# Optimization experiments

Measured on AMD Instinct MI355X. Metric: run time of the kernel, lower is better.

The kernel has to match this reference:

```python
import jax, jax.numpy as jnp
import numpy as np

B, NV, NP, D, K = 8, 2048, 4096, 64, 8  # shapes per batch, vtx/pts counts, feat dim, num_interp
NEG = -1e9


def _unit(x):
    return x / jnp.clip(jnp.linalg.norm(x, axis=-1, keepdims=True), 1e-12)


def _gather(v, idx):
    # v: [B, N, C], idx: [B, Q, K] -> [B, Q, K, C]
    return jax.vmap(lambda a, i: a[i])(v, idx)


def setup_inputs() -> dict:
    key = jax.random.key(0)
    k1, k2, k3, k4, k5 = jax.random.split(key, 5)
    return {
        "vtx": jax.random.normal(k1, (B * NV, 3), jnp.float32),
        "pts": jax.random.normal(k2, (B * NP, 3), jnp.float32),
        "vtx_feature": jax.random.normal(k3, (B * NV, D), jnp.float32),
        "pts_feature": jax.random.normal(k4, (B * NP, D), jnp.float32),
        "vismask_logits": jax.random.normal(k5, (B * NV, 1), jnp.float32),
    }


def reference(vtx, pts, vtx_feature, pts_feature, vismask_logits):
    # --- per-batch min-max normalization of sigmoid(vismask) (serial loop in torch) ---
    vm = jax.nn.sigmoid(vismask_logits).reshape(B, NV, 1)
    vmin = vm.min(axis=1, keepdims=True)
    vmax = vm.max(axis=1, keepdims=True)
    vm = (vm - vmin) / (vmax - vmin)

    vtxb = vtx.reshape(B, NV, 3)
    ptsb = pts.reshape(B, NP, 3)
    vf = vtx_feature.reshape(B, NV, D)
    pf = pts_feature.reshape(B, NP, D)

    # --- cosine KNN: for each vtx, k nearest pts by cosine similarity ---
    sim = jnp.einsum('bnd,bmd->bnm', _unit(vf), _unit(pf))  # [B,NV,NP]
    _, idx = jax.lax.top_k(sim, K)                           # [B,NV,K]

    nbr_pts = _gather(ptsb, idx)                             # [B,NV,K,3]
    nbr_pf = _gather(pf, idx)                                # [B,NV,K,D]
    euclid = nbr_pts - vtxb[:, :, None, :]
    # raw (unnormalized) dot product, weighted by vismask of the query vertex
    fsim = jnp.sum(nbr_pf * vf[:, :, None, :], axis=-1, keepdims=True) * vm[:, :, None, :]
    # scatter_add over assign_index[0] == sum over the K grouped neighbors
    flow_init = jnp.sum(euclid * fsim, axis=2) / jnp.sum(fsim, axis=2)  # [B,NV,3]

    # --- interpolate flow at invisible vertices from visible ones (2nd cosine KNN) ---
    vis = vm >= 0.5                                          # [B,NV,1]
    vfn = _unit(vf)
    sim2 = jnp.einsum('bnd,bmd->bnm', vfn, vfn)              # [B,NV,NV]
    sim2 = jnp.where(vis[:, :, 0][:, None, :], sim2, NEG)    # keys restricted to visible vtx
    _, idx2 = jax.lax.top_k(sim2, K)                         # [B,NV,K]

    nbr_vf = _gather(vf, idx2)                               # [B,NV,K,D]
    nbr_flow = _gather(flow_init, idx2)                      # [B,NV,K,3]
    fsim2 = jnp.sum(nbr_vf * vf[:, :, None, :], axis=-1, keepdims=True)
    invis_flow = jnp.sum(nbr_flow * fsim2, axis=2) / jnp.sum(fsim2, axis=2)

    flow = jnp.where(vis, flow_init, invis_flow)             # flow_init[invis] = invis_flow
    l1_points = jnp.concatenate([flow, vm], axis=-1)         # [B,NV,4]
    return l1_points.reshape(B * NV, 4)
```

## Files before the change

kernel.cpp:

```cpp
#include <hip/hip_runtime.h>
#include <math.h>

#define BB 8
#define NVV 2048
#define NPP 4096
#define DD 64
#define NQ (BB * NVV)
#define QT (NQ / 16)

typedef __attribute__((ext_vector_type(8))) short short8;
typedef __attribute__((ext_vector_type(8))) unsigned short ushort8;
typedef __attribute__((ext_vector_type(4))) float f32x4;


__device__ __forceinline__ unsigned short bf16rn(float x) {
  unsigned u = __float_as_uint(x);
  return (unsigned short)((u + 0x7FFFu + ((u >> 16) & 1u)) >> 16);
}
__device__ __forceinline__ float bf2f(unsigned short h) {
  return __uint_as_float(((unsigned)h) << 16);
}

__device__ __forceinline__ void net8(unsigned* a, unsigned v) {
#pragma unroll
  for (int k = 0; k < 7; k++) {
    unsigned r;
    asm("v_med3_u32 %0, %1, %2, %3" : "=v"(r) : "v"(v), "v"(a[k]), "v"(a[k + 1]));
    a[k] = r;
  }
  a[7] = a[7] > v ? a[7] : v;
}

__device__ __forceinline__ float dot64(const float4* __restrict__ a,
                                       const float4* __restrict__ b) {
  float a0 = 0.f, a1 = 0.f, a2 = 0.f, a3 = 0.f;
#pragma unroll
  for (int c = 0; c < 16; c++) {
    float4 x = a[c], y = b[c];
    a0 = fmaf(x.x, y.x, a0);
    a1 = fmaf(x.y, y.y, a1);
    a2 = fmaf(x.z, y.z, a2);
    a3 = fmaf(x.w, y.w, a3);
  }
  return (a0 + a1) + (a2 + a3);
}

__device__ __forceinline__ unsigned fkey(float s) {
  unsigned u = __float_as_uint(s);
  return ((int)u < 0) ? ~u : (u | 0x80000000u);
}

__global__ __launch_bounds__(256) void k_prep(const float* __restrict__ logits,
                                              const float* __restrict__ vf,
                                              const float* __restrict__ pf,
                                              float* __restrict__ vm,
                                              float* __restrict__ inv_vf_s,
                                              float* __restrict__ inv_pf_s,
                                              unsigned short* __restrict__ vfh,
                                              unsigned short* __restrict__ vfl,
                                              unsigned short* __restrict__ pfh,
                                              unsigned short* __restrict__ pfl,
                                              float* __restrict__ out) {
  int bid = blockIdx.x, t = threadIdx.x;
  if (bid < BB) {
    int b = bid;
    __shared__ float smn[4], smx[4];
    float vals[8];
    float mn = 1e30f, mx = -1e30f;
#pragma unroll
    for (int i = 0; i < 8; i++) {
      float x = logits[b * NVV + t + i * 256];
      float s = 1.0f / (1.0f + expf(-x));
      vals[i] = s;
      mn = fminf(mn, s);
      mx = fmaxf(mx, s);
    }
    for (int o = 32; o; o >>= 1) {
      mn = fminf(mn, __shfl_xor(mn, o, 64));
      mx = fmaxf(mx, __shfl_xor(mx, o, 64));
    }
    int w = t >> 6;
    if ((t & 63) == 0) { smn[w] = mn; smx[w] = mx; }
    __syncthreads();
    mn = fminf(fminf(smn[0], smn[1]), fminf(smn[2], smn[3]));
    mx = fmaxf(fmaxf(smx[0], smx[1]), fmaxf(smx[2], smx[3]));
    float range = mx - mn;
#pragma unroll
    for (int i = 0; i < 8; i++) {
      float v = (vals[i] - mn) / range;
      int g = b * NVV + t + i * 256;
      vm[g] = v;
      out[g * 4 + 3] = v;
    }
  } else {
    int tile_g = (bid - BB) * 4 + (t >> 6);
    int lane = t & 63, c = lane & 15, quad = (lane >> 4) & 3;
    const float* src;
    unsigned short *dh, *dl;
    float* ginv;
    int tile;
    if (tile_g < QT) { tile = tile_g; src = vf; dh = vfh; dl = vfl; ginv = inv_vf_s; }
    else { tile = tile_g - QT; src = pf; dh = pfh; dl = pfl; ginv = inv_pf_s; }
    int row = tile * 16 + c;
    const float* rp = src + (size_t)row * DD + quad * 8;
    float4 a0 = *(const float4*)(rp);
    float4 b0 = *(const float4*)(rp + 4);
    float4 a1 = *(const float4*)(rp + 32);
    float4 b1 = *(const float4*)(rp + 36);
    float xs[16] = {a0.x, a0.y, a0.z, a0.w, b0.x, b0.y, b0.z, b0.w,
                    a1.x, a1.y, a1.z, a1.w, b1.x, b1.y, b1.z, b1.w};
    float ss = 0.f;
#pragma unroll
    for (int j = 0; j < 16; j++) ss = fmaf(xs[j], xs[j], ss);
    ss += __shfl_xor(ss, 16, 64);
    ss += __shfl_xor(ss, 32, 64);
    float inv = 1.0f / fmaxf(sqrtf(ss), 1e-12f);
    if (quad == 0) ginv[row] = 16384.0f * inv;
    ushort8 h, l;
    size_t s0 = (size_t)tile * 128 + lane;
#pragma unroll
    for (int j = 0; j < 8; j++) {
      float xn = xs[j] * inv;
      unsigned short hj = bf16rn(xn);
      h[j] = hj;
      l[j] = bf16rn(xn - bf2f(hj));
    }
    *(ushort8*)(dh + s0 * 8) = h;
    *(ushort8*)(dl + s0 * 8) = l;
#pragma unroll
    for (int j = 0; j < 8; j++) {
      float xn = xs[8 + j] * inv;
      unsigned short hj = bf16rn(xn);
      h[j] = hj;
      l[j] = bf16rn(xn - bf2f(hj));
    }
    *(ushort8*)(dh + (s0 + 64) * 8) = h;
    *(ushort8*)(dl + (s0 + 64) * 8) = l;
  }
}

#define LOADK(d0, d1, d2, d3, KH, KL, tile) do {            \
    size_t bo_ = (size_t)(tile) * 1024 + lane * 8;          \
    d0 = *(const short8*)((KH) + bo_);                      \
    d1 = *(const short8*)((KH) + bo_ + 512);                \
    d2 = *(const short8*)((KL) + bo_);                      \
    d3 = *(const short8*)((KL) + bo_ + 512);                \
  } while (0)

#define MFMA6(c_, h0_, h1_, l0_, l1_) do {                                  \
    c_ = __builtin_amdgcn_mfma_f32_16x16x32_bf16(h0_, qh0, c_, 0, 0, 0);    \
    c_ = __builtin_amdgcn_mfma_f32_16x16x32_bf16(h1_, qh1, c_, 0, 0, 0);    \
    c_ = __builtin_amdgcn_mfma_f32_16x16x32_bf16(h0_, ql0, c_, 0, 0, 0);    \
    c_ = __builtin_amdgcn_mfma_f32_16x16x32_bf16(h1_, ql1, c_, 0, 0, 0);    \
    c_ = __builtin_amdgcn_mfma_f32_16x16x32_bf16(l0_, qh0, c_, 0, 0, 0);    \
    c_ = __builtin_amdgcn_mfma_f32_16x16x32_bf16(l1_, qh1, c_, 0, 0, 0);    \
  } while (0)

#define COMP1(h0_, h1_, l0_, l1_, b16_) do {                                \
    f32x4 c_ = {0.f, 0.f, 0.f, 0.f};                                        \
    MFMA6(c_, h0_, h1_, l0_, l1_);                                          \
    unsigned u0_ = (unsigned)fmaxf(fmaf(c_[0], 520000.0f, 520000.0f), 0.0f);\
    net8(tvA, (u0_ << 12) | (unsigned)((b16_) + 0));                        \
    unsigned u1_ = (unsigned)fmaxf(fmaf(c_[1], 520000.0f, 520000.0f), 0.0f);\
    net8(tvA, (u1_ << 12) | (unsigned)((b16_) + 1));                        \
    unsigned u2_ = (unsigned)fmaxf(fmaf(c_[2], 520000.0f, 520000.0f), 0.0f);\
    net8(tvB, (u2_ << 12) | (unsigned)((b16_) + 2));                        \
    unsigned u3_ = (unsigned)fmaxf(fmaf(c_[3], 520000.0f, 520000.0f), 0.0f);\
    net8(tvB, (u3_ << 12) | (unsigned)((b16_) + 3));                        \
  } while (0)

#define COMP2(h0_, h1_, l0_, l1_, b16_, mp_) do {                           \
    float4 mv_ = *(const float4*)(mp_);                                     \
    f32x4 c_ = {0.f, 0.f, 0.f, 0.f};                                        \
    MFMA6(c_, h0_, h1_, l0_, l1_);                                          \
    unsigned u0_ = (unsigned)fmaxf(fmaf(c_[0], 520000.0f, 520000.0f), 0.0f);\
    unsigned p0_ = (u0_ << 12) | (unsigned)((b16_) + 0);                    \
    net8(tvA, (mv_.x >= 0.5f) ? p0_ : 0u);                                  \
    unsigned u1_ = (unsigned)fmaxf(fmaf(c_[1], 520000.0f, 520000.0f), 0.0f);\
    unsigned p1_ = (u1_ << 12) | (unsigned)((b16_) + 1);                    \
    net8(tvA, (mv_.y >= 0.5f) ? p1_ : 0u);                                  \
    unsigned u2_ = (unsigned)fmaxf(fmaf(c_[2], 520000.0f, 520000.0f), 0.0f);\
    unsigned p2_ = (u2_ << 12) | (unsigned)((b16_) + 2);                    \
    net8(tvB, (mv_.z >= 0.5f) ? p2_ : 0u);                                  \
    unsigned u3_ = (unsigned)fmaxf(fmaf(c_[3], 520000.0f, 520000.0f), 0.0f);\
    unsigned p3_ = (u3_ << 12) | (unsigned)((b16_) + 3);                    \
    net8(tvB, (mv_.w >= 0.5f) ? p3_ : 0u);                                  \
  } while (0)

__global__ __launch_bounds__(256)
void k_knn(const unsigned short* __restrict__ vfh, const unsigned short* __restrict__ vfl,
           const unsigned short* __restrict__ pfh, const unsigned short* __restrict__ pfl,
           const float* __restrict__ vm, unsigned* __restrict__ pc2,
           const float* __restrict__ vf, const float* __restrict__ pf,
           const float* __restrict__ pts, const float* __restrict__ vtx,
           const float* __restrict__ inv_pf_s,
           float* __restrict__ flow_ws, float* __restrict__ out) {
  __shared__ unsigned mg[2][2][16][8];
  __shared__ unsigned cand[16][16];

  int p = blockIdx.x;
  int xcd = p & 7, j = p >> 3;
  int qt_g = xcd * 128 + j;
  int batch = xcd;
  int w = (int)threadIdx.x >> 6;
  int ck = w >> 1, hf = w & 1;
  int lane = threadIdx.x & 63, col = lane & 15, quad = lane >> 4;

  size_t ab = (size_t)qt_g * 1024 + lane * 8;
  short8 qh0 = *(const short8*)(vfh + ab);
  short8 qh1 = *(const short8*)(vfh + ab + 512);
  short8 ql0 = *(const short8*)(vfl + ab);
  short8 ql1 = *(const short8*)(vfl + ab + 512);
  asm volatile("" : "+a"(qh0), "+a"(qh1), "+a"(ql0), "+a"(ql1));

  unsigned tvA[8], tvB[8];

#pragma unroll
  for (int k = 0; k < 8; k++) { tvA[k] = 0u; tvB[k] = 0u; }
  {
    int bt0 = batch * 256 + ck * 128 + hf * 64;
    int tb16 = (ck * 128 + hf * 64) * 16 + quad * 4;
    short8 ah0, ah1, al0, al1, bh0, bh1, bl0, bl1;
    LOADK(ah0, ah1, al0, al1, pfh, pfl, bt0);
#pragma unroll 1
    for (int kt = 0; kt < 62; kt += 2) {
      LOADK(bh0, bh1, bl0, bl1, pfh, pfl, bt0 + kt + 1);
      COMP1(ah0, ah1, al0, al1, tb16 + kt * 16);
      LOADK(ah0, ah1, al0, al1, pfh, pfl, bt0 + kt + 2);
      COMP1(bh0, bh1, bl0, bl1, tb16 + (kt + 1) * 16);
    }
    LOADK(bh0, bh1, bl0, bl1, pfh, pfl, bt0 + 63);
    COMP1(ah0, ah1, al0, al1, tb16 + 62 * 16);
    COMP1(bh0, bh1, bl0, bl1, tb16 + 63 * 16);
  }
#pragma unroll
  for (int k = 0; k < 8; k++) net8(tvA, tvB[k]);
#pragma unroll
  for (int m = 16; m <= 32; m <<= 1) {
    unsigned ov[8];
#pragma unroll
    for (int k = 0; k < 8; k++) ov[k] = (unsigned)__shfl_xor((int)tvA[k], m, 64);
#pragma unroll
    for (int k = 7; k >= 0; k--) net8(tvA, ov[k]);
  }
  if (hf == 1 && quad == 0) {
#pragma unroll
    for (int k = 0; k < 8; k++) mg[0][ck][col][k] = tvA[k];
  }
  __syncthreads();
  if (hf == 0 && quad == 0) {
#pragma unroll
    for (int k = 0; k < 8; k++) net8(tvA, mg[0][ck][col][k]);
#pragma unroll
    for (int k = 0; k < 8; k++)
      cand[col][ck * 8 + k] = tvA[k];
  }
  __syncthreads();

  {
    int t = (int)threadIdx.x;
    int qloc = t >> 4, c = t & 15;
    int q = qt_g * 16 + qloc;
    int base = lane & 48;

    unsigned pk = cand[qloc][c];
    int id = (int)(pk & 0xFFFu);
    int prow = batch * NPP + id;
    const float4* qp = (const float4*)(vf + (size_t)q * DD);
    float dotv = dot64(qp, (const float4*)(pf + (size_t)prow * DD));
    float s = dotv * inv_pf_s[prow];
    unsigned kb = fkey(s);

    int rank = 0;
#pragma unroll
    for (int i = 0; i < 16; i++) {
      unsigned ok = (unsigned)__shfl((int)kb, base + i, 64);
      int oid = __shfl(id, base + i, 64);
      rank += (ok > kb || (ok == kb && oid > id)) ? 1 : 0;
    }
    float wgt = (rank < 8) ? dotv : 0.0f;

    float ax = (pts[prow * 3 + 0] - vtx[q * 3 + 0]) * wgt;
    float ay = (pts[prow * 3 + 1] - vtx[q * 3 + 1]) * wgt;
    float az = (pts[prow * 3 + 2] - vtx[q * 3 + 2]) * wgt;
    float den = wgt;
#pragma unroll
    for (int m = 1; m <= 8; m <<= 1) {
      ax += __shfl_xor(ax, m, 64);
      ay += __shfl_xor(ay, m, 64);
      az += __shfl_xor(az, m, 64);
      den += __shfl_xor(den, m, 64);
    }
    if (c == 0) {
      float fx = ax / den, fy = ay / den, fz = az / den;
      flow_ws[q * 4 + 0] = fx;
      flow_ws[q * 4 + 1] = fy;
      flow_ws[q * 4 + 2] = fz;
      out[q * 4 + 0] = fx;
      out[q * 4 + 1] = fy;
      out[q * 4 + 2] = fz;
    }
  }

#pragma unroll
  for (int k = 0; k < 8; k++) { tvA[k] = 0u; tvB[k] = 0u; }
  {
    const float* mask = vm + batch * NVV;
    int bt0 = batch * 128 + ck * 64 + hf * 32;
    int tbase = ck * 64 + hf * 32;
    int tb16 = tbase * 16 + quad * 4;
    const float* mp0 = mask + tbase * 16 + quad * 4;
    short8 ah0, ah1, al0, al1, bh0, bh1, bl0, bl1;
    LOADK(ah0, ah1, al0, al1, vfh, vfl, bt0);
#pragma unroll 1
    for (int kt = 0; kt < 30; kt += 2) {
      LOADK(bh0, bh1, bl0, bl1, vfh, vfl, bt0 + kt + 1);
      COMP2(ah0, ah1, al0, al1, tb16 + kt * 16, mp0 + kt * 16);
      LOADK(ah0, ah1, al0, al1, vfh, vfl, bt0 + kt + 2);
      COMP2(bh0, bh1, bl0, bl1, tb16 + (kt + 1) * 16, mp0 + (kt + 1) * 16);
    }
    LOADK(bh0, bh1, bl0, bl1, vfh, vfl, bt0 + 31);
    COMP2(ah0, ah1, al0, al1, tb16 + 30 * 16, mp0 + 30 * 16);
    COMP2(bh0, bh1, bl0, bl1, tb16 + 31 * 16, mp0 + 31 * 16);
  }
#pragma unroll
  for (int k = 0; k < 8; k++) net8(tvA, tvB[k]);
#pragma unroll
  for (int m = 16; m <= 32; m <<= 1) {
    unsigned ov[8];
#pragma unroll
    for (int k = 0; k < 8; k++) ov[k] = (unsigned)__shfl_xor((int)tvA[k], m, 64);
#pragma unroll
    for (int k = 7; k >= 0; k--) net8(tvA, ov[k]);
  }
  if (hf == 1 && quad == 0) {
#pragma unroll
    for (int k = 0; k < 8; k++) mg[1][ck][col][k] = tvA[k];
  }
  __syncthreads();
  if (hf == 0 && quad == 0) {
#pragma unroll
    for (int k = 0; k < 8; k++) net8(tvA, mg[1][ck][col][k]);
    int q = qt_g * 16 + col;
#pragma unroll
    for (int k = 0; k < 8; k++)
      pc2[(size_t)(ck * 8 + k) * NQ + q] = tvA[k];
  }
}

__global__ __launch_bounds__(256) void k_merge_final(const unsigned* __restrict__ pc,
                                                     const float* __restrict__ vf,
                                                     const float* __restrict__ vm,
                                                     const float* __restrict__ inv_vf_s,
                                                     const float* __restrict__ flow_ws,
                                                     float* __restrict__ out) {
  int p = blockIdx.x;
  int xcd = p & 7, jj = p >> 3;
  int lb = xcd * 128 + jj;
  int T = lb * 256 + (int)threadIdx.x;
  int q = T >> 4, c = T & 15, batch = q >> 11;
  if (vm[q] >= 0.5f) return;
  int lane = (int)threadIdx.x & 63;
  int base = lane & 48;

  unsigned pk = pc[(size_t)c * NQ + q];
  bool valid = pk > 0xFFFu;
  int id = (int)(pk & 0xFFFu);
  int krow = batch * NVV + id;
  const float4* qp = (const float4*)(vf + (size_t)q * DD);
  float dotv = dot64(qp, (const float4*)(vf + (size_t)krow * DD));
  float s = dotv * inv_vf_s[krow];
  unsigned kb = valid ? fkey(s) : 0u;

  int rank = 0;
#pragma unroll
  for (int i = 0; i < 16; i++) {
    unsigned ok = (unsigned)__shfl((int)kb, base + i, 64);
    int oid = __shfl(id, base + i, 64);
    rank += (ok > kb || (ok == kb && oid > id)) ? 1 : 0;
  }
  float wgt = (valid && rank < 8) ? dotv : 0.0f;

  float ax = flow_ws[krow * 4 + 0] * wgt;
  float ay = flow_ws[krow * 4 + 1] * wgt;
  float az = flow_ws[krow * 4 + 2] * wgt;
  float den = wgt;
#pragma unroll
  for (int m = 1; m <= 8; m <<= 1) {
    ax += __shfl_xor(ax, m, 64);
    ay += __shfl_xor(ay, m, 64);
    az += __shfl_xor(az, m, 64);
    den += __shfl_xor(den, m, 64);
  }
  if (c == 0) {
    out[q * 4 + 0] = ax / den;
    out[q * 4 + 1] = ay / den;
    out[q * 4 + 2] = az / den;
  }
}

extern "C" void kernel_launch(void* const* d_in, const int* in_sizes, int n_in,
                              void* d_out, int out_size, void* d_ws, size_t ws_size,
                              hipStream_t stream) {
  const float* vtx = (const float*)d_in[0];
  const float* pts = (const float*)d_in[1];
  const float* vf = (const float*)d_in[2];
  const float* pf = (const float*)d_in[3];
  const float* lg = (const float*)d_in[4];
  float* out = (float*)d_out;
  float* ws = (float*)d_ws;

  float* vm = ws;
  float* inv_vf_s = ws + 16384;
  float* inv_pf_s = ws + 32768;
  float* flow = ws + 65536;
  unsigned* pc2 = (unsigned*)(ws + 393216);
  unsigned short* vfh = (unsigned short*)(ws + 655360);
  unsigned short* vfl = (unsigned short*)(ws + 1179648);
  unsigned short* pfh = (unsigned short*)(ws + 1703936);
  unsigned short* pfl = (unsigned short*)(ws + 2752512);

  k_prep<<<BB + 768, 256, 0, stream>>>(lg, vf, pf, vm, inv_vf_s, inv_pf_s,
                                       vfh, vfl, pfh, pfl, out);
  k_knn<<<1024, 256, 0, stream>>>(vfh, vfl, pfh, pfl, vm, pc2,
                                  vf, pf, pts, vtx, inv_pf_s, flow, out);
  k_merge_final<<<NQ * 16 / 256, 256, 0, stream>>>(pc2, vf, vm, inv_vf_s,
                                                   flow, out);
}
```

Measured before the change: 163.9 us.

## Fuse prep, KNN and merge kernels into one persistent kernel with grid barriers

Replaces the three kernel launches with a single 512-block persistent kernel. Global atomic-counter barriers separate the normalization/bf16 staging phase, the KNN phase and the invisible-vertex interpolation phase. Each block now handles two query tiles, and the second-KNN candidates stay in shared memory instead of round-tripping through a global buffer. This removes launch gaps and the pc2 traffic, but it adds spin-barrier cost and relies on all 512 blocks being co-resident. It also halves the grid, which may lower parallelism in the KNN phase.

```diff
diff --git a/kernel.cpp b/kernel.cpp
--- a/kernel.cpp
+++ b/kernel.cpp
@@ -50,93 +50,57 @@
   return ((int)u < 0) ? ~u : (u | 0x80000000u);
 }
 
-__global__ __launch_bounds__(256) void k_prep(const float* __restrict__ logits,
-                                              const float* __restrict__ vf,
-                                              const float* __restrict__ pf,
-                                              float* __restrict__ vm,
-                                              float* __restrict__ inv_vf_s,
-                                              float* __restrict__ inv_pf_s,
-                                              unsigned short* __restrict__ vfh,
-                                              unsigned short* __restrict__ vfl,
-                                              unsigned short* __restrict__ pfh,
-                                              unsigned short* __restrict__ pfl,
-                                              float* __restrict__ out) {
-  int bid = blockIdx.x, t = threadIdx.x;
-  if (bid < BB) {
-    int b = bid;
-    __shared__ float smn[4], smx[4];
-    float vals[8];
-    float mn = 1e30f, mx = -1e30f;
-#pragma unroll
-    for (int i = 0; i < 8; i++) {
-      float x = logits[b * NVV + t + i * 256];
-      float s = 1.0f / (1.0f + expf(-x));
-      vals[i] = s;
-      mn = fminf(mn, s);
-      mx = fmaxf(mx, s);
-    }
-    for (int o = 32; o; o >>= 1) {
-      mn = fminf(mn, __shfl_xor(mn, o, 64));
-      mx = fmaxf(mx, __shfl_xor(mx, o, 64));
-    }
-    int w = t >> 6;
-    if ((t & 63) == 0) { smn[w] = mn; smx[w] = mx; }
-    __syncthreads();
-    mn = fminf(fminf(smn[0], smn[1]), fminf(smn[2], smn[3]));
-    mx = fmaxf(fmaxf(smx[0], smx[1]), fmaxf(smx[2], smx[3]));
-    float range = mx - mn;
-#pragma unroll
-    for (int i = 0; i < 8; i++) {
-      float v = (vals[i] - mn) / range;
-      int g = b * NVV + t + i * 256;
-      vm[g] = v;
-      out[g * 4 + 3] = v;
-    }
-  } else {
-    int tile_g = (bid - BB) * 4 + (t >> 6);
-    int lane = t & 63, c = lane & 15, quad = (lane >> 4) & 3;
-    const float* src;
-    unsigned short *dh, *dl;
-    float* ginv;
-    int tile;
-    if (tile_g < QT) { tile = tile_g; src = vf; dh = vfh; dl = vfl; ginv = inv_vf_s; }
-    else { tile = tile_g - QT; src = pf; dh = pfh; dl = pfl; ginv = inv_pf_s; }
-    int row = tile * 16 + c;
-    const float* rp = src + (size_t)row * DD + quad * 8;
-    float4 a0 = *(const float4*)(rp);
-    float4 b0 = *(const float4*)(rp + 4);
-    float4 a1 = *(const float4*)(rp + 32);
-    float4 b1 = *(const float4*)(rp + 36);
-    float xs[16] = {a0.x, a0.y, a0.z, a0.w, b0.x, b0.y, b0.z, b0.w,
-                    a1.x, a1.y, a1.z, a1.w, b1.x, b1.y, b1.z, b1.w};
-    float ss = 0.f;
-#pragma unroll
-    for (int j = 0; j < 16; j++) ss = fmaf(xs[j], xs[j], ss);
-    ss += __shfl_xor(ss, 16, 64);
-    ss += __shfl_xor(ss, 32, 64);
-    float inv = 1.0f / fmaxf(sqrtf(ss), 1e-12f);
-    if (quad == 0) ginv[row] = 16384.0f * inv;
-    ushort8 h, l;
-    size_t s0 = (size_t)tile * 128 + lane;
-#pragma unroll
-    for (int j = 0; j < 8; j++) {
-      float xn = xs[j] * inv;
-      unsigned short hj = bf16rn(xn);
-      h[j] = hj;
-      l[j] = bf16rn(xn - bf2f(hj));
-    }
-    *(ushort8*)(dh + s0 * 8) = h;
-    *(ushort8*)(dl + s0 * 8) = l;
-#pragma unroll
-    for (int j = 0; j < 8; j++) {
-      float xn = xs[8 + j] * inv;
-      unsigned short hj = bf16rn(xn);
-      h[j] = hj;
-      l[j] = bf16rn(xn - bf2f(hj));
-    }
-    *(ushort8*)(dh + (s0 + 64) * 8) = h;
-    *(ushort8*)(dl + (s0 + 64) * 8) = l;
-  }
+__device__ __forceinline__ void gridbar(unsigned* sem, unsigned target) {
+  __syncthreads();
+  __threadfence();
+  if (threadIdx.x == 0) {
+    atomicAdd(sem, 1u);
+    while (atomicAdd(sem, 0u) < target) __builtin_amdgcn_s_sleep(8);
+  }
+  __syncthreads();
+  __threadfence();
+}
+
+__device__ __forceinline__ void stage_tile(const float* __restrict__ src, int tile,
+                                           unsigned short* __restrict__ dh,
+                                           unsigned short* __restrict__ dl,
+                                           float* __restrict__ ginv, int lane) {
+  int c = lane & 15, quad = (lane >> 4) & 3;
+  int row = tile * 16 + c;
+  const float* rp = src + (size_t)row * DD + quad * 8;
+  float4 a0 = *(const float4*)(rp);
+  float4 b0 = *(const float4*)(rp + 4);
+  float4 a1 = *(const float4*)(rp + 32);
+  float4 b1 = *(const float4*)(rp + 36);
+  float xs[16] = {a0.x, a0.y, a0.z, a0.w, b0.x, b0.y, b0.z, b0.w,
+                  a1.x, a1.y, a1.z, a1.w, b1.x, b1.y, b1.z, b1.w};
+  float ss = 0.f;
+#pragma unroll
+  for (int j = 0; j < 16; j++) ss = fmaf(xs[j], xs[j], ss);
+  ss += __shfl_xor(ss, 16, 64);
+  ss += __shfl_xor(ss, 32, 64);
+  float inv = 1.0f / fmaxf(sqrtf(ss), 1e-12f);
+  if (quad == 0) ginv[row] = 16384.0f * inv;
+  ushort8 h, l;
+  size_t s0 = (size_t)tile * 128 + lane;
+#pragma unroll
+  for (int j = 0; j < 8; j++) {
+    float xn = xs[j] * inv;
+    unsigned short hj = bf16rn(xn);
+    h[j] = hj;
+    l[j] = bf16rn(xn - bf2f(hj));
+  }
+  *(ushort8*)(dh + s0 * 8) = h;
+  *(ushort8*)(dl + s0 * 8) = l;
+#pragma unroll
+  for (int j = 0; j < 8; j++) {
+    float xn = xs[8 + j] * inv;
+    unsigned short hj = bf16rn(xn);
+    h[j] = hj;
+    l[j] = bf16rn(xn - bf2f(hj));
+  }
+  *(ushort8*)(dh + (s0 + 64) * 8) = h;
+  *(ushort8*)(dl + (s0 + 64) * 8) = l;
 }
 
 #define LOADK(d0, d1, d2, d3, KH, KL, tile) do {            \
@@ -187,89 +151,234 @@
     net8(tvB, (mv_.w >= 0.5f) ? p3_ : 0u);                                  \
   } while (0)
 
-__global__ __launch_bounds__(256)
-void k_knn(const unsigned short* __restrict__ vfh, const unsigned short* __restrict__ vfl,
-           const unsigned short* __restrict__ pfh, const unsigned short* __restrict__ pfl,
-           const float* __restrict__ vm, unsigned* __restrict__ pc2,
+__global__ __launch_bounds__(256, 4)
+void k_all(const float* __restrict__ vtx, const float* __restrict__ pts,
            const float* __restrict__ vf, const float* __restrict__ pf,
-           const float* __restrict__ pts, const float* __restrict__ vtx,
-           const float* __restrict__ inv_pf_s,
-           float* __restrict__ flow_ws, float* __restrict__ out) {
+           const float* __restrict__ lg, float* __restrict__ out,
+           float* __restrict__ vm, float* __restrict__ inv_vf_s,
+           float* __restrict__ inv_pf_s, float* __restrict__ flow_ws,
+           unsigned short* __restrict__ vfh, unsigned short* __restrict__ vfl,
+           unsigned short* __restrict__ pfh, unsigned short* __restrict__ pfl,
+           unsigned* __restrict__ sem) {
+  __shared__ float smn[2], smx[2];
   __shared__ unsigned mg[2][2][16][8];
   __shared__ unsigned cand[16][16];
+  __shared__ unsigned cand2[2][16][16];
 
   int p = blockIdx.x;
-  int xcd = p & 7, j = p >> 3;
-  int qt_g = xcd * 128 + j;
+  int xcd = p & 7, idx = p >> 3;
   int batch = xcd;
-  int w = (int)threadIdx.x >> 6;
+  int t = (int)threadIdx.x;
+  int w = t >> 6;
   int ck = w >> 1, hf = w & 1;
-  int lane = threadIdx.x & 63, col = lane & 15, quad = lane >> 4;
-
-  size_t ab = (size_t)qt_g * 1024 + lane * 8;
-  short8 qh0 = *(const short8*)(vfh + ab);
-  short8 qh1 = *(const short8*)(vfh + ab + 512);
-  short8 ql0 = *(const short8*)(vfl + ab);
-  short8 ql1 = *(const short8*)(vfl + ab + 512);
-  asm volatile("" : "+a"(qh0), "+a"(qh1), "+a"(ql0), "+a"(ql1));
-
-  unsigned tvA[8], tvB[8];
-
-#pragma unroll
-  for (int k = 0; k < 8; k++) { tvA[k] = 0u; tvB[k] = 0u; }
-  {
-    int bt0 = batch * 256 + ck * 128 + hf * 64;
-    int tb16 = (ck * 128 + hf * 64) * 16 + quad * 4;
-    short8 ah0, ah1, al0, al1, bh0, bh1, bl0, bl1;
-    LOADK(ah0, ah1, al0, al1, pfh, pfl, bt0);
+  int lane = t & 63, col = lane & 15, quad = lane >> 4;
+
+  stage_tile(pf, xcd * 256 + idx * 4 + w, pfh, pfl, inv_pf_s, lane);
+  bool dovm = (idx == 0 && w >= 2);
+  float vals[16];
+  if (w < 2) stage_tile(vf, xcd * 128 + idx * 2 + w, vfh, vfl, inv_vf_s, lane);
+  float mn = 1e30f, mx = -1e30f;
+  if (dovm) {
+    int t2 = t - 128;
+#pragma unroll
+    for (int i = 0; i < 16; i++) {
+      float x = lg[batch * NVV + t2 + i * 128];
+      float s = 1.0f / (1.0f + expf(-x));
+      vals[i] = s;
+      mn = fminf(mn, s);
+      mx = fmaxf(mx, s);
+    }
+    for (int o = 32; o; o >>= 1) {
+      mn = fminf(mn, __shfl_xor(mn, o, 64));
+      mx = fmaxf(mx, __shfl_xor(mx, o, 64));
+    }
+    if (lane == 0) { smn[w - 2] = mn; smx[w - 2] = mx; }
+  }
+  __syncthreads();
+  if (dovm) {
+    int t2 = t - 128;
+    float mnn = fminf(smn[0], smn[1]), mxx = fmaxf(smx[0], smx[1]);
+    float range = mxx - mnn;
+#pragma unroll
+    for (int i = 0; i < 16; i++) {
+      float v = (vals[i] - mnn) / range;
+      int g = batch * NVV + t2 + i * 128;
+      vm[g] = v;
+      out[g * 4 + 3] = v;
+    }
+  }
+
+  gridbar(sem, 512);
+
 #pragma unroll 1
-    for (int kt = 0; kt < 62; kt += 2) {
-      LOADK(bh0, bh1, bl0, bl1, pfh, pfl, bt0 + kt + 1);
-      COMP1(ah0, ah1, al0, al1, tb16 + kt * 16);
-      LOADK(ah0, ah1, al0, al1, pfh, pfl, bt0 + kt + 2);
-      COMP1(bh0, bh1, bl0, bl1, tb16 + (kt + 1) * 16);
-    }
-    LOADK(bh0, bh1, bl0, bl1, pfh, pfl, bt0 + 63);
-    COMP1(ah0, ah1, al0, al1, tb16 + 62 * 16);
-    COMP1(bh0, bh1, bl0, bl1, tb16 + 63 * 16);
-  }
-#pragma unroll
-  for (int k = 0; k < 8; k++) net8(tvA, tvB[k]);
-#pragma unroll
-  for (int m = 16; m <= 32; m <<= 1) {
-    unsigned ov[8];
-#pragma unroll
-    for (int k = 0; k < 8; k++) ov[k] = (unsigned)__shfl_xor((int)tvA[k], m, 64);
-#pragma unroll
-    for (int k = 7; k >= 0; k--) net8(tvA, ov[k]);
-  }
-  if (hf == 1 && quad == 0) {
-#pragma unroll
-    for (int k = 0; k < 8; k++) mg[0][ck][col][k] = tvA[k];
-  }
-  __syncthreads();
-  if (hf == 0 && quad == 0) {
-#pragma unroll
-    for (int k = 0; k < 8; k++) net8(tvA, mg[0][ck][col][k]);
-#pragma unroll
-    for (int k = 0; k < 8; k++)
-      cand[col][ck * 8 + k] = tvA[k];
-  }
-  __syncthreads();
-
-  {
-    int t = (int)threadIdx.x;
+  for (int qi = 0; qi < 2; qi++) {
+    int qt_g = xcd * 128 + idx * 2 + qi;
+
+    size_t ab = (size_t)qt_g * 1024 + lane * 8;
+    short8 qh0 = *(const short8*)(vfh + ab);
+    short8 qh1 = *(const short8*)(vfh + ab + 512);
+    short8 ql0 = *(const short8*)(vfl + ab);
+    short8 ql1 = *(const short8*)(vfl + ab + 512);
+    asm volatile("" : "+a"(qh0), "+a"(qh1), "+a"(ql0), "+a"(ql1));
+
+    unsigned tvA[8], tvB[8];
+
+#pragma unroll
+    for (int k = 0; k < 8; k++) { tvA[k] = 0u; tvB[k] = 0u; }
+    {
+      int bt0 = batch * 256 + ck * 128 + hf * 64;
+      int tb16 = (ck * 128 + hf * 64) * 16 + quad * 4;
+      short8 ah0, ah1, al0, al1, bh0, bh1, bl0, bl1;
+      LOADK(ah0, ah1, al0, al1, pfh, pfl, bt0);
+#pragma unroll 1
+      for (int kt = 0; kt < 62; kt += 2) {
+        LOADK(bh0, bh1, bl0, bl1, pfh, pfl, bt0 + kt + 1);
+        COMP1(ah0, ah1, al0, al1, tb16 + kt * 16);
+        LOADK(ah0, ah1, al0, al1, pfh, pfl, bt0 + kt + 2);
+        COMP1(bh0, bh1, bl0, bl1, tb16 + (kt + 1) * 16);
+      }
+      LOADK(bh0, bh1, bl0, bl1, pfh, pfl, bt0 + 63);
+      COMP1(ah0, ah1, al0, al1, tb16 + 62 * 16);
+      COMP1(bh0, bh1, bl0, bl1, tb16 + 63 * 16);
+    }
+#pragma unroll
+    for (int k = 0; k < 8; k++) net8(tvA, tvB[k]);
+#pragma unroll
+    for (int m = 16; m <= 32; m <<= 1) {
+      unsigned ov[8];
+#pragma unroll
+      for (int k = 0; k < 8; k++) ov[k] = (unsigned)__shfl_xor((int)tvA[k], m, 64);
+#pragma unroll
+      for (int k = 7; k >= 0; k--) net8(tvA, ov[k]);
+    }
+    if (hf == 1 && quad == 0) {
+#pragma unroll
+      for (int k = 0; k < 8; k++) mg[0][ck][col][k] = tvA[k];
+    }
+    __syncthreads();
+    if (hf == 0 && quad == 0) {
+#pragma unroll
+      for (int k = 0; k < 8; k++) net8(tvA, mg[0][ck][col][k]);
+#pragma unroll
+      for (int k = 0; k < 8; k++)
+        cand[col][ck * 8 + k] = tvA[k];
+    }
+
+#pragma unroll
+    for (int k = 0; k < 8; k++) { tvA[k] = 0u; tvB[k] = 0u; }
+    {
+      const float* mask = vm + batch * NVV;
+      int bt0 = batch * 128 + ck * 64 + hf * 32;
+      int tbase = ck * 64 + hf * 32;
+      int tb16 = tbase * 16 + quad * 4;
+      const float* mp0 = mask + tbase * 16 + quad * 4;
+      short8 ah0, ah1, al0, al1, bh0, bh1, bl0, bl1;
+      LOADK(ah0, ah1, al0, al1, vfh, vfl, bt0);
+#pragma unroll 1
+      for (int kt = 0; kt < 30; kt += 2) {
+        LOADK(bh0, bh1, bl0, bl1, vfh, vfl, bt0 + kt + 1);
+        COMP2(ah0, ah1, al0, al1, tb16 + kt * 16, mp0 + kt * 16);
+        LOADK(ah0, ah1, al0, al1, vfh, vfl, bt0 + kt + 2);
+        COMP2(bh0, bh1, bl0, bl1, tb16 + (kt + 1) * 16, mp0 + (kt + 1) * 16);
+      }
+      LOADK(bh0, bh1, bl0, bl1, vfh, vfl, bt0 + 31);
+      COMP2(ah0, ah1, al0, al1, tb16 + 30 * 16, mp0 + 30 * 16);
+      COMP2(bh0, bh1, bl0, bl1, tb16 + 31 * 16, mp0 + 31 * 16);
+    }
+#pragma unroll
+    for (int k = 0; k < 8; k++) net8(tvA, tvB[k]);
+#pragma unroll
+    for (int m = 16; m <= 32; m <<= 1) {
+      unsigned ov[8];
+#pragma unroll
+      for (int k = 0; k < 8; k++) ov[k] = (unsigned)__shfl_xor((int)tvA[k], m, 64);
+#pragma unroll
+      for (int k = 7; k >= 0; k--) net8(tvA, ov[k]);
+    }
+    if (hf == 1 && quad == 0) {
+#pragma unroll
+      for (int k = 0; k < 8; k++) mg[1][ck][col][k] = tvA[k];
+    }
+    __syncthreads();
+    if (hf == 0 && quad == 0) {
+#pragma unroll
+      for (int k = 0; k < 8; k++) net8(tvA, mg[1][ck][col][k]);
+#pragma unroll
+      for (int k = 0; k < 8; k++)
+        cand2[qi][col][ck * 8 + k] = tvA[k];
+    }
+    __syncthreads();
+
+    {
+      int qloc = t >> 4, c = t & 15;
+      int q = qt_g * 16 + qloc;
+      int base = lane & 48;
+
+      unsigned pk = cand[qloc][c];
+      int id = (int)(pk & 0xFFFu);
+      int prow = batch * NPP + id;
+      const float4* qp = (const float4*)(vf + (size_t)q * DD);
+      float dotv = dot64(qp, (const float4*)(pf + (size_t)prow * DD));
+      float s = dotv * inv_pf_s[prow];
+      unsigned kb = fkey(s);
+
+      int rank = 0;
+#pragma unroll
+      for (int i = 0; i < 16; i++) {
+        unsigned ok = (unsigned)__shfl((int)kb, base + i, 64);
+        int oid = __shfl(id, base + i, 64);
+        rank += (ok > kb || (ok == kb && oid > id)) ? 1 : 0;
+      }
+      float wgt = (rank < 8) ? dotv : 0.0f;
+
+      float ax = 0.f, ay = 0.f, az = 0.f, den = 0.f;
+      if (wgt != 0.0f) {
+        ax = (pts[prow * 3 + 0] - vtx[q * 3 + 0]) * wgt;
+        ay = (pts[prow * 3 + 1] - vtx[q * 3 + 1]) * wgt;
+        az = (pts[prow * 3 + 2] - vtx[q * 3 + 2]) * wgt;
+        den = wgt;
+      }
+#pragma unroll
+      for (int m = 1; m <= 8; m <<= 1) {
+        ax += __shfl_xor(ax, m, 64);
+        ay += __shfl_xor(ay, m, 64);
+        az += __shfl_xor(az, m, 64);
+        den += __shfl_xor(den, m, 64);
+      }
+      if (c == 0) {
+        float fx = ax / den, fy = ay / den, fz = az / den;
+        flow_ws[q * 4 + 0] = fx;
+        flow_ws[q * 4 + 1] = fy;
+        flow_ws[q * 4 + 2] = fz;
+        out[q * 4 + 0] = fx;
+        out[q * 4 + 1] = fy;
+        out[q * 4 + 2] = fz;
+      }
+    }
+    __syncthreads();
+  }
+
+  gridbar(sem, 1024);
+
+#pragma unroll 1
+  for (int qi = 0; qi < 2; qi++) {
+    int lb = xcd * 128 + idx * 2 + qi;
     int qloc = t >> 4, c = t & 15;
-    int q = qt_g * 16 + qloc;
+    int q = lb * 16 + qloc;
     int base = lane & 48;
-
-    unsigned pk = cand[qloc][c];
+    bool act = vm[q] < 0.5f;
+
+    unsigned pk = cand2[qi][qloc][c];
+    bool valid = act && (pk > 0xFFFu);
     int id = (int)(pk & 0xFFFu);
-    int prow = batch * NPP + id;
-    const float4* qp = (const float4*)(vf + (size_t)q * DD);
-    float dotv = dot64(qp, (const float4*)(pf + (size_t)prow * DD));
-    float s = dotv * inv_pf_s[prow];
-    unsigned kb = fkey(s);
+    int krow = batch * NVV + id;
+    float dotv = 0.f;
+    unsigned kb = 0u;
+    if (valid) {
+      dotv = dot64((const float4*)(vf + (size_t)q * DD),
+                   (const float4*)(vf + (size_t)krow * DD));
+      kb = fkey(dotv * inv_vf_s[krow]);
+    }
 
     int rank = 0;
 #pragma unroll
@@ -278,12 +387,15 @@
       int oid = __shfl(id, base + i, 64);
       rank += (ok > kb || (ok == kb && oid > id)) ? 1 : 0;
     }
-    float wgt = (rank < 8) ? dotv : 0.0f;
-
-    float ax = (pts[prow * 3 + 0] - vtx[q * 3 + 0]) * wgt;
-    float ay = (pts[prow * 3 + 1] - vtx[q * 3 + 1]) * wgt;
-    float az = (pts[prow * 3 + 2] - vtx[q * 3 + 2]) * wgt;
-    float den = wgt;
+    float wgt = (valid && rank < 8) ? dotv : 0.0f;
+
+    float ax = 0.f, ay = 0.f, az = 0.f, den = 0.f;
+    if (wgt != 0.0f) {
+      ax = flow_ws[krow * 4 + 0] * wgt;
+      ay = flow_ws[krow * 4 + 1] * wgt;
+      az = flow_ws[krow * 4 + 2] * wgt;
+      den = wgt;
+    }
 #pragma unroll
     for (int m = 1; m <= 8; m <<= 1) {
       ax += __shfl_xor(ax, m, 64);
@@ -291,111 +403,11 @@
       az += __shfl_xor(az, m, 64);
       den += __shfl_xor(den, m, 64);
     }
-    if (c == 0) {
-      float fx = ax / den, fy = ay / den, fz = az / den;
-      flow_ws[q * 4 + 0] = fx;
-      flow_ws[q * 4 + 1] = fy;
-      flow_ws[q * 4 + 2] = fz;
-      out[q * 4 + 0] = fx;
-      out[q * 4 + 1] = fy;
-      out[q * 4 + 2] = fz;
-    }
-  }
-
-#pragma unroll
-  for (int k = 0; k < 8; k++) { tvA[k] = 0u; tvB[k] = 0u; }
-  {
-    const float* mask = vm + batch * NVV;
-    int bt0 = batch * 128 + ck * 64 + hf * 32;
-    int tbase = ck * 64 + hf * 32;
-    int tb16 = tbase * 16 + quad * 4;
-    const float* mp0 = mask + tbase * 16 + quad * 4;
-    short8 ah0, ah1, al0, al1, bh0, bh1, bl0, bl1;
-    LOADK(ah0, ah1, al0, al1, vfh, vfl, bt0);
-#pragma unroll 1
-    for (int kt = 0; kt < 30; kt += 2) {
-      LOADK(bh0, bh1, bl0, bl1, vfh, vfl, bt0 + kt + 1);
-      COMP2(ah0, ah1, al0, al1, tb16 + kt * 16, mp0 + kt * 16);
-      LOADK(ah0, ah1, al0, al1, vfh, vfl, bt0 + kt + 2);
-      COMP2(bh0, bh1, bl0, bl1, tb16 + (kt + 1) * 16, mp0 + (kt + 1) * 16);
-    }
-    LOADK(bh0, bh1, bl0, bl1, vfh, vfl, bt0 + 31);
-    COMP2(ah0, ah1, al0, al1, tb16 + 30 * 16, mp0 + 30 * 16);
-    COMP2(bh0, bh1, bl0, bl1, tb16 + 31 * 16, mp0 + 31 * 16);
-  }
-#pragma unroll
-  for (int k = 0; k < 8; k++) net8(tvA, tvB[k]);
-#pragma unroll
-  for (int m = 16; m <= 32; m <<= 1) {
-    unsigned ov[8];
-#pragma unroll
-    for (int k = 0; k < 8; k++) ov[k] = (unsigned)__shfl_xor((int)tvA[k], m, 64);
-#pragma unroll
-    for (int k = 7; k >= 0; k--) net8(tvA, ov[k]);
-  }
-  if (hf == 1 && quad == 0) {
-#pragma unroll
-    for (int k = 0; k < 8; k++) mg[1][ck][col][k] = tvA[k];
-  }
-  __syncthreads();
-  if (hf == 0 && quad == 0) {
-#pragma unroll
-    for (int k = 0; k < 8; k++) net8(tvA, mg[1][ck][col][k]);
-    int q = qt_g * 16 + col;
-#pragma unroll
-    for (int k = 0; k < 8; k++)
-      pc2[(size_t)(ck * 8 + k) * NQ + q] = tvA[k];
-  }
-}
-
-__global__ __launch_bounds__(256) void k_merge_final(const unsigned* __restrict__ pc,
-                                                     const float* __restrict__ vf,
-                                                     const float* __restrict__ vm,
-                                                     const float* __restrict__ inv_vf_s,
-                                                     const float* __restrict__ flow_ws,
-                                                     float* __restrict__ out) {
-  int p = blockIdx.x;
-  int xcd = p & 7, jj = p >> 3;
-  int lb = xcd * 128 + jj;
-  int T = lb * 256 + (int)threadIdx.x;
-  int q = T >> 4, c = T & 15, batch = q >> 11;
-  if (vm[q] >= 0.5f) return;
-  int lane = (int)threadIdx.x & 63;
-  int base = lane & 48;
-
-  unsigned pk = pc[(size_t)c * NQ + q];
-  bool valid = pk > 0xFFFu;
-  int id = (int)(pk & 0xFFFu);
-  int krow = batch * NVV + id;
-  const float4* qp = (const float4*)(vf + (size_t)q * DD);
-  float dotv = dot64(qp, (const float4*)(vf + (size_t)krow * DD));
-  float s = dotv * inv_vf_s[krow];
-  unsigned kb = valid ? fkey(s) : 0u;
-
-  int rank = 0;
-#pragma unroll
-  for (int i = 0; i < 16; i++) {
-    unsigned ok = (unsigned)__shfl((int)kb, base + i, 64);
-    int oid = __shfl(id, base + i, 64);
-    rank += (ok > kb || (ok == kb && oid > id)) ? 1 : 0;
-  }
-  float wgt = (valid && rank < 8) ? dotv : 0.0f;
-
-  float ax = flow_ws[krow * 4 + 0] * wgt;
-  float ay = flow_ws[krow * 4 + 1] * wgt;
-  float az = flow_ws[krow * 4 + 2] * wgt;
-  float den = wgt;
-#pragma unroll
-  for (int m = 1; m <= 8; m <<= 1) {
-    ax += __shfl_xor(ax, m, 64);
-    ay += __shfl_xor(ay, m, 64);
-    az += __shfl_xor(az, m, 64);
-    den += __shfl_xor(den, m, 64);
-  }
-  if (c == 0) {
-    out[q * 4 + 0] = ax / den;
-    out[q * 4 + 1] = ay / den;
-    out[q * 4 + 2] = az / den;
+    if (act && c == 0) {
+      out[q * 4 + 0] = ax / den;
+      out[q * 4 + 1] = ay / den;
+      out[q * 4 + 2] = az / den;
+    }
   }
 }
 
@@ -414,16 +426,13 @@
   float* inv_vf_s = ws + 16384;
   float* inv_pf_s = ws + 32768;
   float* flow = ws + 65536;
-  unsigned* pc2 = (unsigned*)(ws + 393216);
+  unsigned* sem = (unsigned*)(ws + 131072);
   unsigned short* vfh = (unsigned short*)(ws + 655360);
   unsigned short* vfl = (unsigned short*)(ws + 1179648);
   unsigned short* pfh = (unsigned short*)(ws + 1703936);
   unsigned short* pfl = (unsigned short*)(ws + 2752512);
 
-  k_prep<<<BB + 768, 256, 0, stream>>>(lg, vf, pf, vm, inv_vf_s, inv_pf_s,
-                                       vfh, vfl, pfh, pfl, out);
-  k_knn<<<1024, 256, 0, stream>>>(vfh, vfl, pfh, pfl, vm, pc2,
-                                  vf, pf, pts, vtx, inv_pf_s, flow, out);
-  k_merge_final<<<NQ * 16 / 256, 256, 0, stream>>>(pc2, vf, vm, inv_vf_s,
-                                                   flow, out);
-}
+  hipMemsetAsync(sem, 0, 8, stream);
+  k_all<<<512, 256, 0, stream>>>(vtx, pts, vf, pf, lg, out, vm, inv_vf_s,
+                                 inv_pf_s, flow, vfh, vfl, pfh, pfl, sem);
+}
```

New measurement: 383.2 us. 2.34x slower.
